# Kernel optimization log

Measured on AMD Instinct MI355X. Metric: run time of the kernel, lower is better.

The kernel has to match this reference:

```python
import jax, jax.numpy as jnp
import numpy as np

LN_EPS = 1e-5

def _proj(x, w, b):
    # 1x1 conv: x [B,C,H,W], w [O,C], b [O]
    return jnp.einsum('bchw,oc->bohw', x, w) + b[None, :, None, None]

def _layernorm(x, w, b):
    # normalize over last dim
    mu = jnp.mean(x, axis=-1, keepdims=True)
    var = jnp.mean(jnp.square(x - mu), axis=-1, keepdims=True)
    return (x - mu) * jax.lax.rsqrt(var + LN_EPS) * w + b

def setup_inputs() -> dict:
    key = jax.random.key(0)
    ks = jax.random.split(key, 12)
    C = 256
    d = {
        's3': jax.random.normal(ks[0], (2, C, 64, 64), jnp.float32),
        's4': jax.random.normal(ks[1], (2, C, 32, 64), jnp.float32),
        's5': jax.random.normal(ks[2], (2, C, 16, 64), jnp.float32),
        'qw': jax.random.normal(ks[3], (C, C), jnp.float32) * 0.02,
        'qb': jax.random.normal(ks[4], (C,), jnp.float32) * 0.02,
        'kw': jax.random.normal(ks[5], (C, C), jnp.float32) * 0.02,
        'kb': jax.random.normal(ks[6], (C,), jnp.float32) * 0.02,
        'vw': jax.random.normal(ks[7], (C, C), jnp.float32) * 0.02,
        'vb': jax.random.normal(ks[8], (C,), jnp.float32) * 0.02,
        'ow': jax.random.normal(ks[9], (C, C), jnp.float32) * 0.02,
        'ob': jax.random.normal(ks[10], (C,), jnp.float32) * 0.02,
        'ln_w': jnp.ones((C,), jnp.float32),
        'ln_b': jnp.zeros((C,), jnp.float32),
    }
    return d

def reference(s3, s4, s5, qw, qb, kw, kb, vw, vb, ow, ob, ln_w, ln_b):
    B, C, H, W = s3.shape
    num_heads = 8
    head_dim = C // num_heads
    scale = head_dim ** -0.5

    q = _proj(s3, qw, qb).reshape(B, C, H * W)            # [B,C,Nq]
    k4 = _proj(s4, kw, kb).reshape(B, C, -1)
    k5 = _proj(s5, kw, kb).reshape(B, C, -1)
    v4 = _proj(s4, vw, vb).reshape(B, C, -1)
    v5 = _proj(s5, vw, vb).reshape(B, C, -1)
    k = jnp.concatenate([k4, k5], axis=-1)                # [B,C,Nk]
    v = jnp.concatenate([v4, v5], axis=-1)

    # [B,C,N] -> [B,h,N,d]
    def split_heads(t):
        Bn, Cn, N = t.shape
        return t.transpose(0, 2, 1).reshape(Bn, N, num_heads, head_dim).transpose(0, 2, 1, 3)

    qh, kh, vh = split_heads(q), split_heads(k), split_heads(v)
    attn = jnp.einsum('bhqd,bhkd->bhqk', qh, kh) * scale
    attn = jax.nn.softmax(attn, axis=-1)
    out = jnp.einsum('bhqk,bhkd->bhqd', attn, vh)         # [B,h,Nq,d]
    out = out.transpose(0, 2, 1, 3).reshape(B, H * W, C)  # [B,Nq,C]
    out = out.transpose(0, 2, 1).reshape(B, C, H, W)
    out = _proj(out, ow, ob)
    out = s3 + out
    out_flat = out.reshape(B, C, H * W).transpose(0, 2, 1)  # [B,N,C]
    out_flat = _layernorm(out_flat, ln_w, ln_b)
    return out_flat.transpose(0, 2, 1).reshape(B, C, H, W)
```

## Files before the change

### kernel.cpp

```cpp
#include <hip/hip_runtime.h>

typedef __bf16 bf16;
typedef __bf16 bf16x4 __attribute__((ext_vector_type(4)));
typedef __bf16 bf16x8 __attribute__((ext_vector_type(8)));
typedef _Float16 f16;
typedef _Float16 f16x2 __attribute__((ext_vector_type(2)));
typedef _Float16 f16x4 __attribute__((ext_vector_type(4)));
typedef _Float16 f16x8 __attribute__((ext_vector_type(8)));
typedef float f32x4 __attribute__((ext_vector_type(4)));
typedef unsigned int u32x4 __attribute__((ext_vector_type(4)));

#define MFMA16 __builtin_amdgcn_mfma_f32_16x16x32_bf16
#define MFMA16H __builtin_amdgcn_mfma_f32_16x16x32_f16

__device__ __forceinline__ void async16(void* lds, const void* g) {
    __builtin_amdgcn_global_load_lds((const __attribute__((address_space(1))) unsigned int*)g,
                                     (__attribute__((address_space(3))) unsigned int*)lds, 16, 0, 0);
}

__device__ __forceinline__ f16x2 pkrtz(float a, float b) {
    return __builtin_bit_cast(f16x2, __builtin_amdgcn_cvt_pkrtz(a, b));
}

__device__ __forceinline__ float fdot2h(f16x2 a, f16x2 b, float c) {
#if __has_builtin(__builtin_amdgcn_fdot2)
    return __builtin_amdgcn_fdot2(a, b, c, false);
#else
    return c + (float)a[0] * (float)b[0] + (float)a[1] * (float)b[1];
#endif
}

__global__ __launch_bounds__(256) void k_prep(const float* __restrict__ qw, const float* __restrict__ kw,
                                              const float* __restrict__ vw, const float* __restrict__ ow,
                                              bf16* __restrict__ Wb,
                                              const float* __restrict__ s3, const float* __restrict__ s4,
                                              const float* __restrict__ s5,
                                              bf16* __restrict__ s3t, bf16* __restrict__ s45t) {
    __shared__ float T[64][65];
    int bx = blockIdx.x, t = threadIdx.x;
    if (bx < 256) {
        int tt = bx * 256 + t;
        const float* srcs[4] = {qw, kw, vw, ow};
        int which = tt >> 14;
        int idx = (tt & 16383) * 4;
        f32x4 v = *(const f32x4*)(srcs[which] + idx);
        bf16x4 o;
        o[0] = (bf16)v[0]; o[1] = (bf16)v[1]; o[2] = (bf16)v[2]; o[3] = (bf16)v[3];
        *(bf16x4*)(Wb + (size_t)which * 65536 + idx) = o;
        return;
    }
    const float* src; bf16* dst; int N, dstRows, rowOff, x, y, z;
    if (bx < 768)       { int i = bx - 256;  src = s3; dst = s3t;  N = 4096; dstRows = 4096; rowOff = 0;    x = i & 63; y = (i >> 6) & 3; z = i >> 8; }
    else if (bx < 1024) { int i = bx - 768;  src = s4; dst = s45t; N = 2048; dstRows = 3072; rowOff = 0;    x = i & 31; y = (i >> 5) & 3; z = i >> 7; }
    else                { int i = bx - 1024; src = s5; dst = s45t; N = 1024; dstRows = 3072; rowOff = 2048; x = i & 15; y = (i >> 4) & 3; z = i >> 6; }
    int c0 = y * 64, n0 = x * 64, b = z;
    const float* s = src + ((size_t)b * 256 + c0) * N + n0;
#pragma unroll
    for (int i = 0; i < 4; i++) {
        int flat = i * 256 + t;
        int row = flat >> 4;
        int col = (flat & 15) * 4;
        f32x4 v = *(const f32x4*)(s + (size_t)row * N + col);
        T[row][col + 0] = v[0]; T[row][col + 1] = v[1];
        T[row][col + 2] = v[2]; T[row][col + 3] = v[3];
    }
    __syncthreads();
#pragma unroll
    for (int i = 0; i < 4; i++) {
        int flat = i * 256 + t;
        int nrow = flat >> 4;
        int c4 = (flat & 15) * 4;
        bf16x4 o;
        o[0] = (bf16)T[c4 + 0][nrow]; o[1] = (bf16)T[c4 + 1][nrow];
        o[2] = (bf16)T[c4 + 2][nrow]; o[3] = (bf16)T[c4 + 3][nrow];
        *(bf16x4*)(dst + ((size_t)(b * dstRows + rowOff + n0 + nrow)) * 256 + c0 + c4) = o;
    }
}

__global__ __launch_bounds__(256) void k_qkv(const bf16* __restrict__ Wb,
                                             const bf16* __restrict__ s3t, const bf16* __restrict__ s45t,
                                             const float* __restrict__ qb, const float* __restrict__ kb,
                                             const float* __restrict__ vb,
                                             bf16* __restrict__ Qb, bf16* __restrict__ Kb,
                                             f16* __restrict__ Vtb, float qscale) {
    int i = blockIdx.x;
    int mode, n0, m0, b, Nrows;
    const bf16 *A, *Bt; const float* bias; float oscale = 1.0f;
    if (i < 512) {
        mode = 0; A = Wb; Bt = s3t; bias = qb; Nrows = 4096; oscale = qscale;
        n0 = (i & 63) * 64; m0 = ((i >> 6) & 3) * 64; b = i >> 8;
    } else if (i < 896) {
        unsigned j = i - 512;
        mode = 1; A = Wb + 65536; Bt = s45t; bias = kb; Nrows = 3072;
        n0 = (j % 48u) * 64; unsigned rr = j / 48u; m0 = (rr & 3) * 64; b = rr >> 2;
    } else {
        unsigned j = i - 896;
        mode = 2; A = Wb + 131072; Bt = s45t; bias = vb; Nrows = 3072;
        n0 = (j % 48u) * 64; unsigned rr = j / 48u; m0 = (rr & 3) * 64; b = rr >> 2;
    }
    __shared__ __align__(16) bf16 As[2][64 * 32];
    __shared__ __align__(16) bf16 Bs[2][64 * 32];
    int t = threadIdx.x;
    int w = t >> 6, lane = t & 63;
    int lrow = lane & 15, lk = lane >> 4;
    f32x4 acc[4] = {};
    const bf16* Ag = A + (size_t)(m0 + w * 16 + (lane >> 2)) * 256 + (lane & 3) * 8;
    const bf16* Bg = Bt + ((size_t)b * Nrows + n0 + w * 16 + (lane >> 2)) * 256 + (lane & 3) * 8;
    async16(&As[0][w * 512], Ag);
    async16(&Bs[0][w * 512], Bg);
    async16(&As[1][w * 512], Ag + 32);
    async16(&Bs[1][w * 512], Bg + 32);
    for (int s8 = 0; s8 < 8; ++s8) {
        int buf = s8 & 1;
        if (s8 < 7) asm volatile("s_waitcnt vmcnt(2)" ::: "memory");
        else        asm volatile("s_waitcnt vmcnt(0)" ::: "memory");
        __builtin_amdgcn_s_barrier();
        __builtin_amdgcn_sched_barrier(0);
        bf16x8 af = *(const bf16x8*)(&As[buf][(w * 16 + lrow) * 32 + lk * 8]);
#pragma unroll
        for (int ct = 0; ct < 4; ct++) {
            bf16x8 bfr = *(const bf16x8*)(&Bs[buf][(ct * 16 + lrow) * 32 + lk * 8]);
            acc[ct] = MFMA16(af, bfr, acc[ct], 0, 0, 0);
        }
        __builtin_amdgcn_s_barrier();
        if (s8 < 6) {
            async16(&As[buf][w * 512], Ag + (s8 + 2) * 32);
            async16(&Bs[buf][w * 512], Bg + (s8 + 2) * 32);
        }
    }
    int o0 = m0 + w * 16 + lk * 4;
    f32x4 b4 = *(const f32x4*)(bias + o0);
    int head = o0 >> 5;
#pragma unroll
    for (int ct = 0; ct < 4; ct++) {
        int n = n0 + ct * 16 + lrow;
        if (mode == 0) {
            int dd = o0 & 31;
            bf16x4 pv;
#pragma unroll
            for (int j = 0; j < 4; j++) pv[j] = (bf16)((acc[ct][j] + b4[j]) * oscale);
            *(bf16x4*)(Qb + ((size_t)(b * 8 + head) * 4096 + n) * 32 + dd) = pv;
        } else if (mode == 1) {
            int dd = o0 & 31;
            int u = n & 31;
            int np = (n & ~31) | (((u >> 2) & 1) << 4) | ((u >> 3) << 2) | (u & 3);
            bf16x4 pv;
#pragma unroll
            for (int j = 0; j < 4; j++) pv[j] = (bf16)(acc[ct][j] + b4[j]);
            *(bf16x4*)(Kb + ((size_t)(b * 8 + head) * 3072 + np) * 32 + dd) = pv;
        } else {
            int g = (n & 63) >> 3;
#pragma unroll
            for (int j = 0; j < 4; j++) {
                int dd = (o0 & 31) + j;
                int col = (n & ~63) + ((g ^ (dd & 7)) << 3) + (n & 7);
                Vtb[((size_t)(b * 8 + head) * 32 + dd) * 3072 + col] = (f16)(acc[ct][j] + b4[j]);
            }
        }
    }
}

__global__ __launch_bounds__(256, 4) void k_attn(const bf16* __restrict__ Q, const bf16* __restrict__ K,
                                                 const f16* __restrict__ Vt,
                                                 f16* __restrict__ Opart, float* __restrict__ Lsum) {
    int id = blockIdx.x;
    int bh = id & 15;
    int sp = (id >> 4) & 3;
    int q0 = (id >> 6) * 256;
    int kn0 = sp * 768;
    int t = threadIdx.x, w = t >> 6, lane = t & 63;
    int lrow = lane & 15, lk = lane >> 4;
    __shared__ __align__(16) char smem[32768];
    bf16* Ks = (bf16*)smem;
    f16* Vs = (f16*)(smem + 16384);
    f16* Tq = (f16*)smem;
    const bf16* kbase = K + (size_t)bh * 3072 * 32;
    const f16* vbase = Vt + (size_t)bh * 32 * 3072;
    const bf16* kg = kbase + (size_t)(kn0 + w * 16 + (lane >> 2)) * 32 + (lane & 3) * 8;
    const f16* vg = vbase + (size_t)(w * 8 + (lane >> 3)) * 3072 + kn0 + (lane & 7) * 8;
    bf16x8 aq[4];
#pragma unroll
    for (int qg = 0; qg < 4; ++qg)
        aq[qg] = *(const bf16x8*)(Q + ((size_t)bh * 4096 + q0 + w * 64 + qg * 16 + lrow) * 32 + lk * 8);
    f32x4 accO[4][2] = {};
    float lsum[4] = {0.f, 0.f, 0.f, 0.f};
    f32x4 zero = {};
    f16x2 one2; one2[0] = (f16)1.f; one2[1] = (f16)1.f;
    int vkey = lrow & 7;
    async16(Ks + w * 512, kg);
    async16(Ks + 2048 + w * 512, kg + 64 * 32);
    async16(Vs + w * 512, vg);
    async16(Vs + 2048 + w * 512, vg + 64);
    {
        const bf16* kn_ = kg + 128 * 32;
        const f16* vn_ = vg + 128;
        async16(Ks + 4096 + w * 512, kn_);
        async16(Ks + 4096 + 2048 + w * 512, kn_ + 64 * 32);
        async16(Vs + 4096 + w * 512, vn_);
        async16(Vs + 4096 + 2048 + w * 512, vn_ + 64);
    }
    for (int c = 0; c < 6; ++c) {
        int buf = c & 1;
        if (c < 5) asm volatile("s_waitcnt vmcnt(4)" ::: "memory");
        else       asm volatile("s_waitcnt vmcnt(0)" ::: "memory");
        __builtin_amdgcn_s_barrier();
        __builtin_amdgcn_sched_barrier(0);
        const bf16* ksb = Ks + buf * 4096;
        const f16* vsb0 = Vs + buf * 4096;
#pragma unroll
        for (int p = 0; p < 4; ++p) {
            bf16x8 kf0 = *(const bf16x8*)(ksb + (p * 32 + lrow) * 32 + lk * 8);
            bf16x8 kf1 = *(const bf16x8*)(ksb + (p * 32 + 16 + lrow) * 32 + lk * 8);
            const f16* vsb = vsb0 + (p >> 1) * 2048;
            int gran = (((p & 1) << 2) | lk) ^ vkey;
            f16x8 vf0 = *(const f16x8*)(vsb + lrow * 64 + (gran << 3));
            f16x8 vf1 = *(const f16x8*)(vsb + (16 + lrow) * 64 + (gran << 3));
#pragma unroll
            for (int qg = 0; qg < 4; ++qg) {
                f32x4 s0 = MFMA16(kf0, aq[qg], zero, 0, 0, 0);
                f32x4 s1 = MFMA16(kf1, aq[qg], zero, 0, 0, 0);
                f16x2 h0 = pkrtz(__builtin_amdgcn_exp2f(s0[0]), __builtin_amdgcn_exp2f(s0[1]));
                f16x2 h1 = pkrtz(__builtin_amdgcn_exp2f(s0[2]), __builtin_amdgcn_exp2f(s0[3]));
                f16x2 h2 = pkrtz(__builtin_amdgcn_exp2f(s1[0]), __builtin_amdgcn_exp2f(s1[1]));
                f16x2 h3 = pkrtz(__builtin_amdgcn_exp2f(s1[2]), __builtin_amdgcn_exp2f(s1[3]));
                f16x8 pk;
                pk[0] = h0[0]; pk[1] = h0[1]; pk[2] = h1[0]; pk[3] = h1[1];
                pk[4] = h2[0]; pk[5] = h2[1]; pk[6] = h3[0]; pk[7] = h3[1];
                lsum[qg] = fdot2h(h0, one2, lsum[qg]);
                lsum[qg] = fdot2h(h1, one2, lsum[qg]);
                lsum[qg] = fdot2h(h2, one2, lsum[qg]);
                lsum[qg] = fdot2h(h3, one2, lsum[qg]);
                accO[qg][0] = MFMA16H(vf0, pk, accO[qg][0], 0, 0, 0);
                accO[qg][1] = MFMA16H(vf1, pk, accO[qg][1], 0, 0, 0);
            }
        }
        __builtin_amdgcn_s_barrier();
        if (c < 4) {
            const bf16* kn_ = kg + (size_t)(c + 2) * 128 * 32;
            const f16* vn_ = vg + (c + 2) * 128;
            async16(Ks + buf * 4096 + w * 512, kn_);
            async16(Ks + buf * 4096 + 2048 + w * 512, kn_ + 64 * 32);
            async16(Vs + buf * 4096 + w * 512, vn_);
            async16(Vs + buf * 4096 + 2048 + w * 512, vn_ + 64);
        }
    }
    int sb = sp * 16 + bh;
#pragma unroll
    for (int qg = 0; qg < 4; ++qg) {
        lsum[qg] += __shfl_xor(lsum[qg], 16, 64);
        lsum[qg] += __shfl_xor(lsum[qg], 32, 64);
    }
    if (lane < 16) {
#pragma unroll
        for (int qg = 0; qg < 4; ++qg)
            Lsum[(size_t)sb * 4096 + q0 + w * 64 + qg * 16 + lane] = lsum[qg];
    }
    f16* tw = Tq + w * 2112;
#pragma unroll
    for (int qg = 0; qg < 4; ++qg)
#pragma unroll
        for (int dh = 0; dh < 2; ++dh)
#pragma unroll
            for (int i = 0; i < 4; ++i)
                tw[(dh * 16 + lk * 4 + i) * 66 + qg * 16 + lrow] = (f16)accO[qg][dh][i];
    int q4 = (lane & 15) * 4, dgrp = (lane >> 4) * 8;
#pragma unroll
    for (int qq = 0; qq < 4; ++qq) {
        f16x8 ov;
#pragma unroll
        for (int dj = 0; dj < 8; ++dj) ov[dj] = tw[(dgrp + dj) * 66 + q4 + qq];
        *(f16x8*)(Opart + ((size_t)sb * 4096 + q0 + w * 64 + q4 + qq) * 32 + dgrp) = ov;
    }
}

__global__ __launch_bounds__(256) void k_oln(const bf16* __restrict__ A, const f16* __restrict__ Opart,
                                             const float* __restrict__ Ls, const float* __restrict__ bias,
                                             const bf16* __restrict__ s3t,
                                             const float* __restrict__ lnw, const float* __restrict__ lnb,
                                             float* __restrict__ out) {
    int i = blockIdx.x;
    int b = i >> 7, n0 = (i & 127) * 32;
    __shared__ __align__(16) char smem[34176];
    bf16* As = (bf16*)smem;
    bf16* Bs = (bf16*)(smem + 20480);
    float* T = (float*)smem;
    float* ps = (float*)(smem + 32896);
    float* pq = (float*)(smem + 33408);
    float* mu_s = (float*)(smem + 33920);
    float* rs_s = (float*)(smem + 34048);
    int t = threadIdx.x, w = t >> 6, lane = t & 63;
    int lrow = lane & 15, lk = lane >> 4;
    f32x4 acc[4][2] = {};
    int rB = t >> 3, cgB = (t & 7) * 4;
    int q = n0 + rB;
    const size_t SPS = (size_t)16 * 4096 * 32;
    for (int kc = 0; kc < 256; kc += 32) {
        int bh = b * 8 + (kc >> 5);
        const bf16* ar = A + (size_t)t * 256 + kc;
        u32x4 va0 = *(const u32x4*)(ar);
        u32x4 va1 = *(const u32x4*)(ar + 8);
        u32x4 va2 = *(const u32x4*)(ar + 16);
        u32x4 va3 = *(const u32x4*)(ar + 24);
        float l = 0.f;
#pragma unroll
        for (int sp = 0; sp < 4; ++sp) l += Ls[(size_t)(sp * 16 + bh) * 4096 + q];
        float rl = 1.0f / l;
        const f16* obp = Opart + ((size_t)bh * 4096 + q) * 32 + cgB;
        f32x4 sv = {};
#pragma unroll
        for (int sp = 0; sp < 4; ++sp) {
            f16x4 av = *(const f16x4*)(obp + sp * SPS);
#pragma unroll
            for (int j = 0; j < 4; ++j) sv[j] += (float)av[j];
        }
        bf16x4 bb;
#pragma unroll
        for (int j = 0; j < 4; ++j) bb[j] = (bf16)(sv[j] * rl);
        *(u32x4*)(As + t * 40 + 0) = va0;
        *(u32x4*)(As + t * 40 + 8) = va1;
        *(u32x4*)(As + t * 40 + 16) = va2;
        *(u32x4*)(As + t * 40 + 24) = va3;
        *(bf16x4*)(Bs + rB * 40 + cgB) = bb;
        __syncthreads();
#pragma unroll
        for (int mt = 0; mt < 4; ++mt) {
            bf16x8 af = *(const bf16x8*)(As + (mt * 64 + w * 16 + lrow) * 40 + lk * 8);
#pragma unroll
            for (int ct = 0; ct < 2; ++ct) {
                bf16x8 bfr = *(const bf16x8*)(Bs + (ct * 16 + lrow) * 40 + lk * 8);
                acc[mt][ct] = MFMA16(af, bfr, acc[mt][ct], 0, 0, 0);
            }
        }
        __syncthreads();
    }
    float wsum[2] = {0.f, 0.f}, wsq[2] = {0.f, 0.f};
#pragma unroll
    for (int ct = 0; ct < 2; ++ct) {
        int n = ct * 16 + lrow;
#pragma unroll
        for (int mt = 0; mt < 4; ++mt) {
            int c0 = mt * 64 + w * 16 + lk * 4;
            f32x4 b4 = *(const f32x4*)(bias + c0);
            bf16x4 rv = *(const bf16x4*)(s3t + ((size_t)b * 4096 + n0 + n) * 256 + c0);
#pragma unroll
            for (int j = 0; j < 4; ++j) {
                float v = acc[mt][ct][j] + b4[j] + (float)rv[j];
                T[n * 257 + c0 + j] = v;
                wsum[ct] += v;
                wsq[ct] += v * v;
            }
        }
    }
#pragma unroll
    for (int ct = 0; ct < 2; ++ct) {
        wsum[ct] += __shfl_xor(wsum[ct], 16, 64);
        wsum[ct] += __shfl_xor(wsum[ct], 32, 64);
        wsq[ct] += __shfl_xor(wsq[ct], 16, 64);
        wsq[ct] += __shfl_xor(wsq[ct], 32, 64);
    }
    if (lk == 0) {
#pragma unroll
        for (int ct = 0; ct < 2; ++ct) {
            ps[w * 32 + ct * 16 + lrow] = wsum[ct];
            pq[w * 32 + ct * 16 + lrow] = wsq[ct];
        }
    }
    __syncthreads();
    if (t < 32) {
        float S = ps[t] + ps[32 + t] + ps[64 + t] + ps[96 + t];
        float Q2 = pq[t] + pq[32 + t] + pq[64 + t] + pq[96 + t];
        float m = S * (1.0f / 256.0f);
        mu_s[t] = m;
        rs_s[t] = rsqrtf(Q2 * (1.0f / 256.0f) - m * m + 1e-5f);
    }
    __syncthreads();
    int cb = t >> 3, n4 = (t & 7) * 4;
#pragma unroll
    for (int cc8 = 0; cc8 < 8; ++cc8) {
        int c = cb + cc8 * 32;
        float wv = lnw[c], bv = lnb[c];
        f32x4 o;
#pragma unroll
        for (int k2 = 0; k2 < 4; ++k2)
            o[k2] = (T[(n4 + k2) * 257 + c] - mu_s[n4 + k2]) * rs_s[n4 + k2] * wv + bv;
        *(f32x4*)(out + ((size_t)b * 256 + c) * 4096 + n0 + n4) = o;
    }
}

extern "C" void kernel_launch(void* const* d_in, const int* in_sizes, int n_in,
                              void* d_out, int out_size, void* d_ws, size_t ws_size,
                              hipStream_t stream) {
    const float* s3  = (const float*)d_in[0];
    const float* s4  = (const float*)d_in[1];
    const float* s5  = (const float*)d_in[2];
    const float* qw  = (const float*)d_in[3];
    const float* qb  = (const float*)d_in[4];
    const float* kw  = (const float*)d_in[5];
    const float* kb  = (const float*)d_in[6];
    const float* vw  = (const float*)d_in[7];
    const float* vb  = (const float*)d_in[8];
    const float* ow  = (const float*)d_in[9];
    const float* ob  = (const float*)d_in[10];
    const float* lnw = (const float*)d_in[11];
    const float* lnb = (const float*)d_in[12];
    float* out = (float*)d_out;
    char* ws = (char*)d_ws;

    bf16* Wb    = (bf16*)(ws);
    bf16* s3t   = (bf16*)(ws + (512ull << 10));
    bf16* s45t  = (bf16*)(ws + (4608ull << 10));
    bf16* Qb    = (bf16*)(ws + (7680ull << 10));
    bf16* Kb    = Qb + (2ull * 8 * 4096 * 32);
    f16*  Vtb   = (f16*)(Kb + (2ull * 8 * 3072 * 32));
    f16*  Opart = (f16*)(ws + (17920ull << 10));
    float* Lsum = (float*)(ws + (34304ull << 10));

    const float qscale = 0.17677669529663688f * 1.4426950408889634f;

    k_prep<<<1152, 256, 0, stream>>>(qw, kw, vw, ow, Wb, s3, s4, s5, s3t, s45t);
    k_qkv<<<1280, 256, 0, stream>>>(Wb, s3t, s45t, qb, kb, vb, Qb, Kb, Vtb, qscale);
    k_attn<<<1024, 256, 0, stream>>>(Qb, Kb, Vtb, Opart, Lsum);
    k_oln<<<256, 256, 0, stream>>>(Wb + 196608, Opart, Lsum, ob, s3t, lnw, lnb, out);
}
```

Before: 144.4 us.

## Pipeline output-projection weight loads asynchronously and vectorize V transpose stores

In the projection kernel's V mode, the MFMA operands are swapped so each lane holds a row of output channels, which lets the transposed, swizzled V tile be written as 4-wide f16 vector stores instead of scalar stores. In the fused output-projection plus LayerNorm kernel, all eight head partial sums are combined and normalized into a full-K LDS tile once up front. The weight tiles are then streamed with double-buffered async global-to-LDS loads behind the MFMA loop, replacing the per-step synchronous loads and two __syncthreads. This raises LDS use to about 50KB per block, which may reduce occupancy.

```diff
diff --git a/kernel.cpp b/kernel.cpp
--- a/kernel.cpp
+++ b/kernel.cpp
@@ -120,7 +120,8 @@
 #pragma unroll
         for (int ct = 0; ct < 4; ct++) {
             bf16x8 bfr = *(const bf16x8*)(&Bs[buf][(ct * 16 + lrow) * 32 + lk * 8]);
-            acc[ct] = MFMA16(af, bfr, acc[ct], 0, 0, 0);
+            if (mode == 2) acc[ct] = MFMA16(bfr, af, acc[ct], 0, 0, 0);
+            else           acc[ct] = MFMA16(af, bfr, acc[ct], 0, 0, 0);
         }
         __builtin_amdgcn_s_barrier();
         if (s8 < 6) {
@@ -128,33 +129,43 @@
             async16(&Bs[buf][w * 512], Bg + (s8 + 2) * 32);
         }
     }
-    int o0 = m0 + w * 16 + lk * 4;
-    f32x4 b4 = *(const f32x4*)(bias + o0);
-    int head = o0 >> 5;
-#pragma unroll
-    for (int ct = 0; ct < 4; ct++) {
-        int n = n0 + ct * 16 + lrow;
-        if (mode == 0) {
-            int dd = o0 & 31;
-            bf16x4 pv;
-#pragma unroll
-            for (int j = 0; j < 4; j++) pv[j] = (bf16)((acc[ct][j] + b4[j]) * oscale);
-            *(bf16x4*)(Qb + ((size_t)(b * 8 + head) * 4096 + n) * 32 + dd) = pv;
-        } else if (mode == 1) {
-            int dd = o0 & 31;
-            int u = n & 31;
-            int np = (n & ~31) | (((u >> 2) & 1) << 4) | ((u >> 3) << 2) | (u & 3);
-            bf16x4 pv;
-#pragma unroll
-            for (int j = 0; j < 4; j++) pv[j] = (bf16)(acc[ct][j] + b4[j]);
-            *(bf16x4*)(Kb + ((size_t)(b * 8 + head) * 3072 + np) * 32 + dd) = pv;
-        } else {
-            int g = (n & 63) >> 3;
-#pragma unroll
-            for (int j = 0; j < 4; j++) {
-                int dd = (o0 & 31) + j;
-                int col = (n & ~63) + ((g ^ (dd & 7)) << 3) + (n & 7);
-                Vtb[((size_t)(b * 8 + head) * 32 + dd) * 3072 + col] = (f16)(acc[ct][j] + b4[j]);
+    if (mode == 2) {
+        int o = m0 + w * 16 + lrow;
+        int head = o >> 5;
+        int dd = o & 31;
+        float bs = bias[o];
+        int key = dd & 7;
+        f16* vrow = Vtb + ((size_t)(b * 8 + head) * 32 + dd) * 3072;
+#pragma unroll
+        for (int ct = 0; ct < 4; ct++) {
+            int g = ct * 2 + (lk >> 1);
+            int col = n0 + ((g ^ key) << 3) + (lk & 1) * 4;
+            f16x4 pv;
+#pragma unroll
+            for (int j = 0; j < 4; j++) pv[j] = (f16)(acc[ct][j] + bs);
+            *(f16x4*)(vrow + col) = pv;
+        }
+    } else {
+        int o0 = m0 + w * 16 + lk * 4;
+        f32x4 b4 = *(const f32x4*)(bias + o0);
+        int head = o0 >> 5;
+#pragma unroll
+        for (int ct = 0; ct < 4; ct++) {
+            int n = n0 + ct * 16 + lrow;
+            if (mode == 0) {
+                int dd = o0 & 31;
+                bf16x4 pv;
+#pragma unroll
+                for (int j = 0; j < 4; j++) pv[j] = (bf16)((acc[ct][j] + b4[j]) * oscale);
+                *(bf16x4*)(Qb + ((size_t)(b * 8 + head) * 4096 + n) * 32 + dd) = pv;
+            } else {
+                int dd = o0 & 31;
+                int u = n & 31;
+                int np = (n & ~31) | (((u >> 2) & 1) << 4) | ((u >> 3) << 2) | (u & 3);
+                bf16x4 pv;
+#pragma unroll
+                for (int j = 0; j < 4; j++) pv[j] = (bf16)(acc[ct][j] + b4[j]);
+                *(bf16x4*)(Kb + ((size_t)(b * 8 + head) * 3072 + np) * 32 + dd) = pv;
             }
         }
     }
@@ -280,59 +291,75 @@
                                              float* __restrict__ out) {
     int i = blockIdx.x;
     int b = i >> 7, n0 = (i & 127) * 32;
-    __shared__ __align__(16) char smem[34176];
+    __shared__ __align__(16) char smem[50944];
     bf16* As = (bf16*)smem;
-    bf16* Bs = (bf16*)(smem + 20480);
+    bf16* Bs = (bf16*)(smem + 32768);
     float* T = (float*)smem;
-    float* ps = (float*)(smem + 32896);
-    float* pq = (float*)(smem + 33408);
-    float* mu_s = (float*)(smem + 33920);
-    float* rs_s = (float*)(smem + 34048);
+    float* ps = (float*)(smem + 49664);
+    float* pq = (float*)(smem + 50176);
+    float* mu_s = (float*)(smem + 50688);
+    float* rs_s = (float*)(smem + 50816);
     int t = threadIdx.x, w = t >> 6, lane = t & 63;
     int lrow = lane & 15, lk = lane >> 4;
     f32x4 acc[4][2] = {};
-    int rB = t >> 3, cgB = (t & 7) * 4;
-    int q = n0 + rB;
     const size_t SPS = (size_t)16 * 4096 * 32;
-    for (int kc = 0; kc < 256; kc += 32) {
-        int bh = b * 8 + (kc >> 5);
-        const bf16* ar = A + (size_t)t * 256 + kc;
-        u32x4 va0 = *(const u32x4*)(ar);
-        u32x4 va1 = *(const u32x4*)(ar + 8);
-        u32x4 va2 = *(const u32x4*)(ar + 16);
-        u32x4 va3 = *(const u32x4*)(ar + 24);
-        float l = 0.f;
-#pragma unroll
-        for (int sp = 0; sp < 4; ++sp) l += Ls[(size_t)(sp * 16 + bh) * 4096 + q];
-        float rl = 1.0f / l;
-        const f16* obp = Opart + ((size_t)bh * 4096 + q) * 32 + cgB;
-        f32x4 sv = {};
-#pragma unroll
-        for (int sp = 0; sp < 4; ++sp) {
-            f16x4 av = *(const f16x4*)(obp + sp * SPS);
-#pragma unroll
-            for (int j = 0; j < 4; ++j) sv[j] += (float)av[j];
-        }
-        bf16x4 bb;
-#pragma unroll
-        for (int j = 0; j < 4; ++j) bb[j] = (bf16)(sv[j] * rl);
-        *(u32x4*)(As + t * 40 + 0) = va0;
-        *(u32x4*)(As + t * 40 + 8) = va1;
-        *(u32x4*)(As + t * 40 + 16) = va2;
-        *(u32x4*)(As + t * 40 + 24) = va3;
-        *(bf16x4*)(Bs + rB * 40 + cgB) = bb;
-        __syncthreads();
-#pragma unroll
-        for (int mt = 0; mt < 4; ++mt) {
-            bf16x8 af = *(const bf16x8*)(As + (mt * 64 + w * 16 + lrow) * 40 + lk * 8);
-#pragma unroll
-            for (int ct = 0; ct < 2; ++ct) {
-                bf16x8 bfr = *(const bf16x8*)(Bs + (ct * 16 + lrow) * 40 + lk * 8);
+#define STAGE_A(buf_, kc_)                                                              \
+    {                                                                                   \
+        _Pragma("unroll")                                                               \
+        for (int s_ = 0; s_ < 4; ++s_) {                                                \
+            int f_ = (w * 4 + s_) * 64 + lane;                                          \
+            async16(As + (buf_) * 8192 + f_ * 8,                                        \
+                    A + (size_t)(f_ >> 2) * 256 + (kc_) + (f_ & 3) * 8);                \
+        }                                                                               \
+    }
+    STAGE_A(0, 0)
+    STAGE_A(1, 32)
+    {
+        int rB = t >> 3;
+        int q = n0 + rB;
+        int c4 = (t & 7) * 4;
+#pragma unroll
+        for (int cg8 = 0; cg8 < 8; ++cg8) {
+            int bh = b * 8 + cg8;
+            float l = 0.f;
+#pragma unroll
+            for (int sp = 0; sp < 4; ++sp) l += Ls[(size_t)(sp * 16 + bh) * 4096 + q];
+            float rl = 1.0f / l;
+            const f16* obp = Opart + ((size_t)bh * 4096 + q) * 32 + c4;
+            f32x4 sv = {};
+#pragma unroll
+            for (int sp = 0; sp < 4; ++sp) {
+                f16x4 av = *(const f16x4*)(obp + sp * SPS);
+#pragma unroll
+                for (int j = 0; j < 4; ++j) sv[j] += (float)av[j];
+            }
+            bf16x4 bb;
+#pragma unroll
+            for (int j = 0; j < 4; ++j) bb[j] = (bf16)(sv[j] * rl);
+            *(bf16x4*)(Bs + rB * 264 + cg8 * 32 + c4) = bb;
+        }
+    }
+    asm volatile("s_waitcnt lgkmcnt(0)" ::: "memory");
+    for (int s8 = 0; s8 < 8; ++s8) {
+        int buf = s8 & 1;
+        int kc = s8 * 32;
+        if (s8 < 7) asm volatile("s_waitcnt vmcnt(4)" ::: "memory");
+        else        asm volatile("s_waitcnt vmcnt(0)" ::: "memory");
+        __builtin_amdgcn_s_barrier();
+        __builtin_amdgcn_sched_barrier(0);
+#pragma unroll
+        for (int ct = 0; ct < 2; ++ct) {
+            bf16x8 bfr = *(const bf16x8*)(Bs + (ct * 16 + lrow) * 264 + kc + lk * 8);
+#pragma unroll
+            for (int mt = 0; mt < 4; ++mt) {
+                bf16x8 af = *(const bf16x8*)(As + buf * 8192 + (mt * 64 + w * 16 + lrow) * 32 + lk * 8);
                 acc[mt][ct] = MFMA16(af, bfr, acc[mt][ct], 0, 0, 0);
             }
         }
-        __syncthreads();
-    }
+        __builtin_amdgcn_s_barrier();
+        if (s8 < 6) STAGE_A(buf, (s8 + 2) * 32)
+    }
+#undef STAGE_A
     float wsum[2] = {0.f, 0.f}, wsq[2] = {0.f, 0.f};
 #pragma unroll
     for (int ct = 0; ct < 2; ++ct) {
```

Result: no change. 142.8 us (-1.1%).
